# Kernel tuning notes

Measured on AMD Instinct MI355X. Metric: run time of the kernel, lower is better.

The kernel has to match this reference:

```python
import jax, jax.numpy as jnp
import numpy as np

B = 32768      # batch of head nodes
E = 1048576    # total edges (avg degree ~32)
DIM = 64
N_H, N_R, N_T = 3846, 60, 9366


def setup_inputs() -> dict:
    key = jax.random.key(0)
    k = jax.random.split(key, 7)
    h = jax.random.randint(k[0], (B,), 0, N_H)
    edge_seg = jnp.sort(jax.random.randint(k[1], (E,), 0, B))
    edge_rel = jax.random.randint(k[2], (E,), 0, N_R)
    edge_tail = jax.random.randint(k[3], (E,), 0, N_T)
    H_emb = jax.random.normal(k[4], (N_H, DIM), dtype=jnp.float32)
    R_emb = jax.random.normal(k[5], (N_R, DIM), dtype=jnp.float32)
    T_emb = jax.random.normal(k[6], (N_T, DIM), dtype=jnp.float32)
    return {"h": h, "edge_seg": edge_seg, "edge_rel": edge_rel,
            "edge_tail": edge_tail, "H_emb": H_emb, "R_emb": R_emb,
            "T_emb": T_emb}


def reference(h, edge_seg, edge_rel, edge_tail, H_emb, R_emb, T_emb):
    # Per-head embedding, gathered out to each of its edges.  [E, DIM]
    Hs = H_emb[h][edge_seg]
    R_v = R_emb[edge_rel]                  # [E, DIM]
    # Attention logits: dot(H_v[j], R_v[k]) per edge.  [E]
    scores = jnp.sum(Hs * R_v, axis=-1)
    # Segment (per-head) softmax over the ragged neighbor lists.
    m = jax.ops.segment_max(scores, edge_seg, num_segments=B)
    m = jnp.where(jnp.isfinite(m), m, jnp.float32(0.0))  # guard empty segs
    e = jnp.exp(scores - m[edge_seg])
    denom = jax.ops.segment_sum(e, edge_seg, num_segments=B)
    w = e / jnp.where(denom > 0, denom, jnp.float32(1.0))[edge_seg]
    # Original: Hv = (T_v - R_v) * score; V_New = sum over ALL elements
    # (a scalar), written into the whole row v_c[j].  Equivalently:
    contrib = w * jnp.sum(T_emb[edge_tail] - R_v, axis=-1)   # [E]
    vc_scalar = jax.ops.segment_sum(contrib, edge_seg, num_segments=B)  # [B]
    return jnp.broadcast_to(vc_scalar[:, None], (B, DIM))
```

## Files before the change

### kernel.cpp

```cpp
#include <hip/hip_runtime.h>
#include <math.h>


__global__ __launch_bounds__(256) void setup_k(
    const float* __restrict__ H, const float* __restrict__ R,
    const float* __restrict__ T,
    float* __restrict__ P, float* __restrict__ tsum, float* __restrict__ rsumg,
    int NH, int NR, int NT, int sBlocks)
{
    int b   = blockIdx.x;
    int tid = threadIdx.x;

    if (b < sBlocks) {
        __shared__ float Rt[64 * 64];
        for (int t = tid; t < NR * 64; t += 256) {
            int r = t >> 6, d = t & 63;
            Rt[d * NR + r] = R[t];
        }
        __syncthreads();
        if (b == 0 && tid < NR) {
            float s = 0.f;
            #pragma unroll 8
            for (int d = 0; d < 64; ++d) s += Rt[d * NR + tid];
            rsumg[tid] = s;
        }

        int idx = b * 256 + tid;
        if (idx < NH * NR) {
            int i = idx / NR;
            int r = idx - i * NR;
            const float4* h4 = (const float4*)(H + (size_t)i * 64);
            float acc = 0.f;
            #pragma unroll
            for (int q = 0; q < 16; ++q) {
                float4 hv = h4[q];
                int d = q * 4;
                acc = fmaf(hv.x, Rt[(d + 0) * NR + r], acc);
                acc = fmaf(hv.y, Rt[(d + 1) * NR + r], acc);
                acc = fmaf(hv.z, Rt[(d + 2) * NR + r], acc);
                acc = fmaf(hv.w, Rt[(d + 3) * NR + r], acc);
            }
            P[idx] = __expf(acc);
        }
        return;
    }
    b -= sBlocks;

    {
        int lane = tid & 63;
        int row  = b * 16 + (tid >> 6) * 4 + (lane >> 4);
        if (row < NT) {
            float4 v = ((const float4*)T)[(size_t)row * 16 + (lane & 15)];
            float s = v.x + v.y + v.z + v.w;
            s += __shfl_xor(s, 8, 64);
            s += __shfl_xor(s, 4, 64);
            s += __shfl_xor(s, 2, 64);
            s += __shfl_xor(s, 1, 64);
            if ((lane & 15) == 0) tsum[row] = s;
        }
    }
}

__global__ __launch_bounds__(256) void main_k(
    const int* __restrict__ h, const int* __restrict__ eseg,
    const int* __restrict__ edge_rel, const int* __restrict__ edge_tail,
    const float* __restrict__ P, const float* __restrict__ tsum,
    const float* __restrict__ rsumg,
    float* __restrict__ out, int B, int E, int NR)
{
    __shared__ int   bounds[33];
    __shared__ float rs[64];
    int tid  = threadIdx.x;
    int base = blockIdx.x * 32;

    if (tid < NR) rs[tid] = rsumg[tid];
    if (tid < 33) {
        int s = base + tid;
        int lo = 0, hi = E;
        while (lo < hi) {
            int mid = (lo + hi) >> 1;
            if (eseg[mid] < s) lo = mid + 1; else hi = mid;
        }
        bounds[tid] = lo;
    }
    __syncthreads();

    int sub  = tid & 31;
    int gidx = tid >> 5;
    #pragma unroll
    for (int k = 0; k < 4; ++k) {
        int j   = gidx + k * 8;
        int grp = base + j;
        if (grp >= B) break;
        int lo = bounds[j];
        int hi = bounds[j + 1];
        const float* Prow = P + (size_t)h[grp] * NR;

        float se = 0.f, sec = 0.f;
        for (int e = lo + sub; e < hi; e += 32) {
            int rel = edge_rel[e];
            int tl  = edge_tail[e];
            float pv = Prow[rel];
            float c  = tsum[tl] - rs[rel];
            sec = fmaf(pv, c, sec);
            se += pv;
        }
        #pragma unroll
        for (int off = 16; off; off >>= 1) {
            se  += __shfl_xor(se, off, 64);
            sec += __shfl_xor(sec, off, 64);
        }
        float vc = (se > 0.f) ? (sec / se) : 0.f;
        *(float2*)(out + (size_t)grp * 64 + sub * 2) = make_float2(vc, vc);
    }
}

extern "C" void kernel_launch(void* const* d_in, const int* in_sizes, int n_in,
                              void* d_out, int out_size, void* d_ws, size_t ws_size,
                              hipStream_t stream)
{
    const int*   h     = (const int*)d_in[0];
    const int*   eseg  = (const int*)d_in[1];
    const int*   erel  = (const int*)d_in[2];
    const int*   etail = (const int*)d_in[3];
    const float* Hv    = (const float*)d_in[4];
    const float* Rv    = (const float*)d_in[5];
    const float* Tv    = (const float*)d_in[6];

    int B  = in_sizes[0];
    int E  = in_sizes[1];
    int NH = in_sizes[4] / 64;
    int NR = in_sizes[5] / 64;
    int NT = in_sizes[6] / 64;

    char*  ws  = (char*)d_ws;
    size_t off = 0;
    auto alloc = [&](size_t bytes) -> void* {
        void* q = ws + off;
        off = (off + bytes + 255) & ~(size_t)255;
        return q;
    };
    float* P     = (float*)alloc((size_t)NH * NR * sizeof(float));
    float* tsum  = (float*)alloc((size_t)NT * sizeof(float));
    float* rsumg = (float*)alloc(64 * sizeof(float));
    (void)ws_size;

    int sBlocks = (NH * NR + 255) / 256;
    int tBlocks = (NT + 15) / 16;
    setup_k<<<sBlocks + tBlocks, 256, 0, stream>>>(
        Hv, Rv, Tv, P, tsum, rsumg, NH, NR, NT, sBlocks);

    main_k<<<(B + 31) / 32, 256, 0, stream>>>(
        h, eseg, erel, etail, P, tsum, rsumg, (float*)d_out, B, E, NR);
}
```

Baseline: 23.30 us.

## Fuse setup and main kernels, computing P and tail sums per block in LDS

```diff
diff --git a/kernel.cpp b/kernel.cpp
--- a/kernel.cpp
+++ b/kernel.cpp
@@ -2,106 +2,117 @@
 #include <math.h>
 
 
-__global__ __launch_bounds__(256) void setup_k(
+#define RT_S 61
+#define CAP  2048
+
+__global__ __launch_bounds__(256) void fused_k(
+    const int* __restrict__ h, const int* __restrict__ eseg,
+    const int* __restrict__ erel, const int* __restrict__ etail,
     const float* __restrict__ H, const float* __restrict__ R,
-    const float* __restrict__ T,
-    float* __restrict__ P, float* __restrict__ tsum, float* __restrict__ rsumg,
-    int NH, int NR, int NT, int sBlocks)
+    const float* __restrict__ T, float* __restrict__ out,
+    int B, int E, int NR)
 {
-    int b   = blockIdx.x;
-    int tid = threadIdx.x;
+    __shared__ float Rt[64 * RT_S];
+    __shared__ float P_lds[2048];
+    __shared__ float c_lds[CAP];
+    __shared__ float rs[64];
+    __shared__ int   bounds[33];
+    __shared__ int   h_lds[32];
 
-    if (b < sBlocks) {
-        __shared__ float Rt[64 * 64];
-        for (int t = tid; t < NR * 64; t += 256) {
-            int r = t >> 6, d = t & 63;
-            Rt[d * NR + r] = R[t];
+    const int tid  = threadIdx.x;
+    const int base = blockIdx.x * 32;
+
+    if (tid < 32 && base + tid < B) h_lds[tid] = h[base + tid];
+    for (int t = tid; t < NR * 64; t += 256) {
+        int r = t >> 6, d = t & 63;
+        Rt[d * RT_S + r] = R[t];
+    }
+    __syncthreads();
+
+    if (tid >= 223) {
+        int s = base + tid - 223;
+        int lo = 0, hi = E;
+        while (lo < hi) {
+            int mid = (lo + hi) >> 1;
+            if (eseg[mid] < s) lo = mid + 1; else hi = mid;
         }
-        __syncthreads();
-        if (b == 0 && tid < NR) {
+        bounds[tid - 223] = lo;
+    } else {
+        if (tid < NR) {
             float s = 0.f;
-            #pragma unroll 8
-            for (int d = 0; d < 64; ++d) s += Rt[d * NR + tid];
-            rsumg[tid] = s;
+            for (int d = 0; d < 64; ++d) s += Rt[d * RT_S + tid];
+            rs[tid] = s;
         }
-
-        int idx = b * 256 + tid;
-        if (idx < NH * NR) {
-            int i = idx / NR;
-            int r = idx - i * NR;
-            const float4* h4 = (const float4*)(H + (size_t)i * 64);
+        const int tot = 32 * NR;
+        for (int t = tid; t < tot; t += 223) {
+            int j = t / NR, r = t - j * NR;
+            const float4* h4 = (const float4*)(H + (size_t)h_lds[j] * 64);
             float acc = 0.f;
             #pragma unroll
             for (int q = 0; q < 16; ++q) {
                 float4 hv = h4[q];
                 int d = q * 4;
-                acc = fmaf(hv.x, Rt[(d + 0) * NR + r], acc);
-                acc = fmaf(hv.y, Rt[(d + 1) * NR + r], acc);
-                acc = fmaf(hv.z, Rt[(d + 2) * NR + r], acc);
-                acc = fmaf(hv.w, Rt[(d + 3) * NR + r], acc);
+                acc = fmaf(hv.x, Rt[(d + 0) * RT_S + r], acc);
+                acc = fmaf(hv.y, Rt[(d + 1) * RT_S + r], acc);
+                acc = fmaf(hv.z, Rt[(d + 2) * RT_S + r], acc);
+                acc = fmaf(hv.w, Rt[(d + 3) * RT_S + r], acc);
             }
-            P[idx] = __expf(acc);
+            P_lds[t] = __expf(acc);
         }
-        return;
     }
-    b -= sBlocks;
+    __syncthreads();
+
+    const int eLo = bounds[0];
+    const int eHi = bounds[32];
 
     {
-        int lane = tid & 63;
-        int row  = b * 16 + (tid >> 6) * 4 + (lane >> 4);
-        if (row < NT) {
-            float4 v = ((const float4*)T)[(size_t)row * 16 + (lane & 15)];
-            float s = v.x + v.y + v.z + v.w;
+        int wave = tid >> 6, lane = tid & 63;
+        int g = lane >> 4, l16 = lane & 15;
+        int nCap = min(eHi, eLo + CAP);
+        for (int e4 = eLo + wave * 4; e4 < nCap; e4 += 16) {
+            int e = e4 + g;
+            float s = 0.f;
+            if (e < nCap) {
+                int tl = etail[e];
+                float4 v = ((const float4*)T)[(size_t)tl * 16 + l16];
+                s = v.x + v.y + v.z + v.w;
+            }
             s += __shfl_xor(s, 8, 64);
             s += __shfl_xor(s, 4, 64);
             s += __shfl_xor(s, 2, 64);
             s += __shfl_xor(s, 1, 64);
-            if ((lane & 15) == 0) tsum[row] = s;
+            if (l16 == 0 && e < nCap) c_lds[e - eLo] = s;
         }
-    }
-}
-
-__global__ __launch_bounds__(256) void main_k(
-    const int* __restrict__ h, const int* __restrict__ eseg,
-    const int* __restrict__ edge_rel, const int* __restrict__ edge_tail,
-    const float* __restrict__ P, const float* __restrict__ tsum,
-    const float* __restrict__ rsumg,
-    float* __restrict__ out, int B, int E, int NR)
-{
-    __shared__ int   bounds[33];
-    __shared__ float rs[64];
-    int tid  = threadIdx.x;
-    int base = blockIdx.x * 32;
-
-    if (tid < NR) rs[tid] = rsumg[tid];
-    if (tid < 33) {
-        int s = base + tid;
-        int lo = 0, hi = E;
-        while (lo < hi) {
-            int mid = (lo + hi) >> 1;
-            if (eseg[mid] < s) lo = mid + 1; else hi = mid;
-        }
-        bounds[tid] = lo;
     }
     __syncthreads();
 
-    int sub  = tid & 31;
-    int gidx = tid >> 5;
+    int sub = tid & 31, gidx = tid >> 5;
     #pragma unroll
     for (int k = 0; k < 4; ++k) {
         int j   = gidx + k * 8;
         int grp = base + j;
         if (grp >= B) break;
-        int lo = bounds[j];
-        int hi = bounds[j + 1];
-        const float* Prow = P + (size_t)h[grp] * NR;
+        int lo = bounds[j], hi = bounds[j + 1];
+        const float* Pj = P_lds + j * NR;
 
         float se = 0.f, sec = 0.f;
         for (int e = lo + sub; e < hi; e += 32) {
-            int rel = edge_rel[e];
-            int tl  = edge_tail[e];
-            float pv = Prow[rel];
-            float c  = tsum[tl] - rs[rel];
+            int rel  = erel[e];
+            float pv = Pj[rel];
+            float c;
+            int ci = e - eLo;
+            if (ci < CAP) c = c_lds[ci];
+            else {
+                const float4* t4 = (const float4*)(T + (size_t)etail[e] * 64);
+                float4 a = t4[0];
+                #pragma unroll
+                for (int q = 1; q < 16; ++q) {
+                    float4 v = t4[q];
+                    a.x += v.x; a.y += v.y; a.z += v.z; a.w += v.w;
+                }
+                c = a.x + a.y + a.z + a.w;
+            }
+            c -= rs[rel];
             sec = fmaf(pv, c, sec);
             se += pv;
         }
@@ -129,27 +140,9 @@
 
     int B  = in_sizes[0];
     int E  = in_sizes[1];
-    int NH = in_sizes[4] / 64;
     int NR = in_sizes[5] / 64;
-    int NT = in_sizes[6] / 64;
+    (void)d_ws; (void)ws_size; (void)n_in; (void)out_size;
 
-    char*  ws  = (char*)d_ws;
-    size_t off = 0;
-    auto alloc = [&](size_t bytes) -> void* {
-        void* q = ws + off;
-        off = (off + bytes + 255) & ~(size_t)255;
-        return q;
-    };
-    float* P     = (float*)alloc((size_t)NH * NR * sizeof(float));
-    float* tsum  = (float*)alloc((size_t)NT * sizeof(float));
-    float* rsumg = (float*)alloc(64 * sizeof(float));
-    (void)ws_size;
-
-    int sBlocks = (NH * NR + 255) / 256;
-    int tBlocks = (NT + 15) / 16;
-    setup_k<<<sBlocks + tBlocks, 256, 0, stream>>>(
-        Hv, Rv, Tv, P, tsum, rsumg, NH, NR, NT, sBlocks);
-
-    main_k<<<(B + 31) / 32, 256, 0, stream>>>(
-        h, eseg, erel, etail, P, tsum, rsumg, (float*)d_out, B, E, NR);
+    fused_k<<<(B + 31) / 32, 256, 0, stream>>>(
+        h, eseg, erel, etail, Hv, Rv, Tv, (float*)d_out, B, E, NR);
 }
```

After: 72.89 us. 3.13x slower.
